# Performance work log

Measured on AMD Instinct MI355X. Metric: run time of the kernel, lower is better.

Reference implementation:

```python
import jax, jax.numpy as jnp
import numpy as np

N = 131072        # total nodes
D = 256           # d_model (params.emb_dim)
STEPS = 16        # depth steps
G = N // STEPS    # nodes per depth step (equal-sized groups)
B = 16            # batch (number of trees); all lengths equal N//B
V = 1024          # len(id2word)
# op schedule: -1 leaf embedding, -2 numeric encoder, 0/1 unary ('sin','cos'), 2/3 binary ('add','mul')
SCHEDULE = [-1, -2, 0, 2, 1, 3, 0, 2, 1, 3, 0, 2, 1, 3, 0, 2]


def setup_inputs() -> dict:
    key = jax.random.key(0)
    ks = jax.random.split(key, 8)
    tokens = jax.random.randint(ks[0], (N,), 0, V, dtype=jnp.int32)
    # children of a node at depth d must already be computed: indices < d*G
    rng = np.random.default_rng(0)
    li = np.zeros(N, np.int32)
    ri = np.zeros(N, np.int32)
    for d in range(2, STEPS):
        li[d * G:(d + 1) * G] = rng.integers(0, d * G, G)
        ri[d * G:(d + 1) * G] = rng.integers(0, d * G, G)
    depths = jnp.repeat(jnp.arange(STEPS, dtype=jnp.int32), G)
    operation_order = jnp.array(SCHEDULE, dtype=jnp.int32)
    lengths = jnp.full((B,), N // B, dtype=jnp.int32)
    s = 0.05
    leaf_table = jax.random.normal(ks[1], (V, D), jnp.float32)
    num_W1 = jax.random.normal(ks[2], (D, 1), jnp.float32) * s
    num_b1 = jnp.zeros((D,), jnp.float32)
    num_W2 = jax.random.normal(ks[3], (D, D), jnp.float32) * s
    num_b2 = jnp.zeros((D,), jnp.float32)
    una_W = jax.random.normal(ks[4], (2, 4, D, D), jnp.float32) * s
    una_b = jnp.zeros((2, 4, D), jnp.float32)
    bin_W = jax.random.normal(ks[5], (2, 10, D, D), jnp.float32) * s
    bin_b = jnp.zeros((2, 5, D), jnp.float32)
    return dict(tokens=tokens, left_idx=jnp.asarray(li), right_idx=jnp.asarray(ri),
                depths=depths, operation_order=operation_order, lengths=lengths,
                leaf_table=leaf_table, num_W1=num_W1, num_b1=num_b1,
                num_W2=num_W2, num_b2=num_b2,
                una_W=una_W, una_b=una_b, bin_W=bin_W, bin_b=bin_b)


def _unary_cell(hc, W, b):
    # hc: [G, 2, D]; W: [4, D, D] (data, forget, output, input); b: [4, D]
    h, c = hc[:, 0], hc[:, 1]
    g = jnp.einsum('nd,ked->kne', h, W) + b[:, None, :]  # y = h @ W_k.T + b_k
    i = jax.nn.sigmoid(g[0])
    f = jax.nn.sigmoid(g[1])
    o = jax.nn.sigmoid(g[2])
    u = jnp.tanh(g[3])
    c2 = i * u + f * c
    h2 = o * jnp.tanh(c2)
    h2 = h2 / jnp.linalg.norm(h2)  # global (Frobenius) norm, as in torch h.norm(p=2)
    c2 = c2 / jnp.linalg.norm(c2)
    return jnp.stack([h2, c2], axis=1)


def _binary_cell(hcl, hcr, W, b):
    # W: [10, D, D] = (data_l, data_r, f_ll, f_lr, f_rl, f_rr, out_l, out_r, in_l, in_r)
    # b: [5, D] = (data, forget_l, forget_r, output, input)
    hl, cl = hcl[:, 0], hcl[:, 1]
    hr, cr = hcr[:, 0], hcr[:, 1]
    gl = jnp.einsum('nd,ked->kne', hl, W[jnp.array([0, 2, 4, 6, 8])])
    gr = jnp.einsum('nd,ked->kne', hr, W[jnp.array([1, 3, 5, 7, 9])])
    g = gl + gr + b[:, None, :]
    i = jax.nn.sigmoid(g[0])
    f_l = jax.nn.sigmoid(g[1])
    f_r = jax.nn.sigmoid(g[2])
    o = jax.nn.sigmoid(g[3])
    u = jnp.tanh(g[4])
    c2 = i * u + f_l * cl + f_r * cr
    h2 = o * jnp.tanh(c2)
    h2 = h2 / jnp.linalg.norm(h2)
    c2 = c2 / jnp.linalg.norm(c2)
    return jnp.stack([h2, c2], axis=1)


def reference(tokens, left_idx, right_idx, depths, operation_order, lengths,
              leaf_table, num_W1, num_b1, num_W2, num_b2,
              una_W, una_b, bin_W, bin_b):
    sched = np.asarray(operation_order).tolist()  # static dispatch schedule
    n = tokens.shape[0]
    steps = len(sched)
    g = n // steps
    d_model = leaf_table.shape[1]
    acts = jnp.zeros((n, 2, d_model), leaf_table.dtype)
    for d, op in enumerate(sched):
        s = d * g
        if op == -1:  # leaf embedding with max_norm=1.0 renorm (non-differentiable scale)
            e = leaf_table[tokens[s:s + g]]
            nrm = jnp.linalg.norm(e, axis=-1, keepdims=True)
            scale = jax.lax.stop_gradient(jnp.minimum(1.0, 1.0 / (nrm + 1e-7)))
            e = e * scale
            step_act = jnp.stack([e, jnp.zeros_like(e)], axis=1)
        elif op == -2:  # numeric encoder
            x = tokens[s:s + g].astype(leaf_table.dtype)[:, None]
            h1 = jax.nn.sigmoid(x @ num_W1.T + num_b1)
            e = jax.nn.sigmoid(h1 @ num_W2.T + num_b2)
            step_act = jnp.stack([e, jnp.zeros_like(e)], axis=1)
        elif op in (0, 1):  # unary LSTM cell: gather child then cell
            child = acts[left_idx[s:s + g]]
            step_act = _unary_cell(child, una_W[op], una_b[op])
        else:  # binary LSTM cell: gather both children
            l = acts[left_idx[s:s + g]]
            r = acts[right_idx[s:s + g]]
            step_act = _binary_cell(l, r, bin_W[op - 2], bin_b[op - 2])
        acts = jax.lax.dynamic_update_slice(acts, step_act, (s, 0, 0))
    hidden = acts[:, 0, :]  # [N, D]
    batch = lengths.shape[0]
    # all lengths equal -> pad_sequence is a reshape: [B, L, D]
    return hidden.reshape(batch, n // batch, d_model)
```

## Files before the change

### kernel.cpp

```cpp
#include <hip/hip_runtime.h>
#include <hip/hip_bf16.h>
#include <cstdint>

typedef unsigned short u16;
typedef unsigned int u32;
typedef __attribute__((ext_vector_type(4))) float floatx4;
typedef __attribute__((ext_vector_type(8))) short shortx8;

#define G_STEP 8192
#define N_TOTAL 131072
#define RHALF (1280*256)

__device__ __forceinline__ float bfu2f(u16 x){ return __uint_as_float(((unsigned)x)<<16); }
__device__ __forceinline__ u16 f2bfu(float x){ __hip_bfloat16 b = __float2bfloat16(x); return *reinterpret_cast<u16*>(&b); }
__device__ __forceinline__ float sigm(float x){ return 1.0f/(1.0f+__expf(-x)); }
__device__ __forceinline__ float tanh_(float x){
  float cx = fminf(fmaxf(x,-15.f),15.f);
  float e = __expf(2.f*cx);
  return (e-1.f)/(e+1.f);
}
__device__ __forceinline__ float invs(float x){ return 1.0f/sqrtf(x); }

__device__ __forceinline__ void gl16(const void* g, void* l){
  __builtin_amdgcn_global_load_lds((const __attribute__((address_space(1))) u32*)g,
                                   (__attribute__((address_space(3))) u32*)l, 16, 0, 0);
}

template<int V> __device__ __forceinline__ void wait_vm();
template<> __device__ __forceinline__ void wait_vm<0>(){ asm volatile("s_waitcnt vmcnt(0)" ::: "memory"); }
template<> __device__ __forceinline__ void wait_vm<8>(){ asm volatile("s_waitcnt vmcnt(8)" ::: "memory"); }
template<> __device__ __forceinline__ void wait_vm<9>(){ asm volatile("s_waitcnt vmcnt(9)" ::: "memory"); }
__device__ __forceinline__ void wait_lgkm0(){ asm volatile("s_waitcnt lgkmcnt(0)" ::: "memory"); }

__device__ __forceinline__ void cvt8(const float* __restrict__ src, u16* __restrict__ dst){
  float4 a = *reinterpret_cast<const float4*>(src);
  float4 b = *reinterpret_cast<const float4*>(src+4);
  ushort4 o0; o0.x=f2bfu(a.x); o0.y=f2bfu(a.y); o0.z=f2bfu(a.z); o0.w=f2bfu(a.w);
  ushort4 o1; o1.x=f2bfu(b.x); o1.y=f2bfu(b.y); o1.z=f2bfu(b.z); o1.w=f2bfu(b.w);
  *reinterpret_cast<ushort4*>(dst)   = o0;
  *reinterpret_cast<ushort4*>(dst+4) = o1;
}

__global__ __launch_bounds__(256) void setup_kernel(
    const int* __restrict__ tokens, const float* __restrict__ leaf_table,
    const float* __restrict__ W1, const float* __restrict__ b1,
    const float* __restrict__ una_W, const float* __restrict__ bin_W,
    const float* __restrict__ num_W2,
    u16* __restrict__ wbu, u16* __restrict__ wbb, u16* __restrict__ wbn,
    u16* __restrict__ h1, u16* __restrict__ H, u16* __restrict__ C,
    float* __restrict__ sumsq)
{
  const int b = blockIdx.x, tid = threadIdx.x;
  if (b < 256){
    int row = b*8 + (tid>>5), d0 = (tid&31)*8;
    int op = row>>10, w = row&1023;
    int gate = (w>>4)&3, e = ((w>>6)<<4) | (w&15);
    cvt8(una_W + (size_t)((op*4+gate)*256 + e)*256 + d0, wbu + (size_t)row*256 + d0);
  } else if (b < 896){
    int row = (b-256)*8 + (tid>>5), d0 = (tid&31)*8;
    int ob = row / 2560, rem = row - ob*2560;
    int lr = rem / 1280, rw = rem - lr*1280;
    int eblk = rw / 80, rem2 = rw - eblk*80;
    int gate = rem2 >> 4, el = rem2 & 15;
    int e = eblk*16 + el;
    cvt8(bin_W + (size_t)((ob*10 + 2*gate + lr)*256 + e)*256 + d0, wbb + (size_t)row*256 + d0);
  } else if (b < 928){
    int row = (b-896)*8 + (tid>>5), d0 = (tid&31)*8;
    cvt8(num_W2 + (size_t)row*256 + d0, wbn + (size_t)row*256 + d0);
  } else if (b < 2976){
    int wave = tid >> 6, lane = tid & 63;
    int node = (b-928)*4 + wave;
    int t = tokens[node];
    const float4 e4 = *reinterpret_cast<const float4*>(leaf_table + (size_t)t*256 + lane*4);
    float ss = e4.x*e4.x + e4.y*e4.y + e4.z*e4.z + e4.w*e4.w;
    #pragma unroll
    for (int o = 32; o; o >>= 1) ss += __shfl_down(ss, o);
    ss = __shfl(ss, 0);
    float scale = fminf(1.0f, 1.0f/(sqrtf(ss) + 1e-7f));
    ushort4 hv;
    hv.x = f2bfu(e4.x*scale); hv.y = f2bfu(e4.y*scale);
    hv.z = f2bfu(e4.z*scale); hv.w = f2bfu(e4.w*scale);
    ushort4 zv; zv.x = zv.y = zv.z = zv.w = 0;
    *reinterpret_cast<ushort4*>(H + (size_t)node*256 + lane*4) = hv;
    *reinterpret_cast<ushort4*>(C + (size_t)node*256 + lane*4) = zv;
  } else if (b < 4000){
    int flat = (b-2976)*2048 + tid*8;
    int n = flat >> 8, d0 = flat & 255;
    float x = (float)tokens[G_STEP + n];
    float4 w0 = *reinterpret_cast<const float4*>(W1 + d0);
    float4 w1 = *reinterpret_cast<const float4*>(W1 + d0 + 4);
    float4 c0 = *reinterpret_cast<const float4*>(b1 + d0);
    float4 c1 = *reinterpret_cast<const float4*>(b1 + d0 + 4);
    ushort4 o0, o1;
    o0.x = f2bfu(sigm(x*w0.x + c0.x)); o0.y = f2bfu(sigm(x*w0.y + c0.y));
    o0.z = f2bfu(sigm(x*w0.z + c0.z)); o0.w = f2bfu(sigm(x*w0.w + c0.w));
    o1.x = f2bfu(sigm(x*w1.x + c1.x)); o1.y = f2bfu(sigm(x*w1.y + c1.y));
    o1.z = f2bfu(sigm(x*w1.z + c1.z)); o1.w = f2bfu(sigm(x*w1.w + c1.w));
    *reinterpret_cast<ushort4*>(h1 + flat)     = o0;
    *reinterpret_cast<ushort4*>(h1 + flat + 4) = o1;
  } else {
    if (tid < 32) sumsq[tid] = ((tid & 15) < 2) ? 1.0f : 0.0f;
  }
}

template<int MODE>
__global__ __launch_bounds__(256, 2) void gemm_fused(
    const u16* __restrict__ Asrc, const int* __restrict__ lidx,
    const int* __restrict__ ridx, const u16* __restrict__ Wb,
    const float* __restrict__ bias, const u16* __restrict__ Cin,
    float* __restrict__ sumsq, u16* __restrict__ H, u16* __restrict__ C,
    int sbase, int step)
{
  constexpr int NG  = (MODE==0) ? 1 : (MODE==1 ? 4 : 5);
  constexpr int NBR = (MODE==2) ? 160 : 128;
  constexpr int NT  = (MODE==2) ? 8 : 4;
  constexpr int BR  = NBR/32;
  constexpr int WN  = (MODE==2) ? 80 : 64;
  constexpr int NFR = WN/16;
  constexpr int LPS = 4 + BR;

  __shared__ u16 SA[2][128][64];
  __shared__ u16 SB[2][NBR][64];
  __shared__ float scH[16];
  __shared__ float scC[16];
  __shared__ float red[8];

  const int tid  = threadIdx.x;
  const int lane = tid & 63, wave = tid >> 6;

  const int bid = blockIdx.x;
  const int j   = bid >> 3;
  const int bx  = (bid & 7) + 8*(j & 7);
  const int by  = j >> 3;

  const int mbase = bx*128;
  const int nbase = by*NBR;
  const int l15 = lane & 15, kg = lane >> 4;
  const int rhi = lane >> 3;
  const int lc  = (lane & 7) ^ rhi;

  if (MODE != 0){
    if (tid < 16)           scH[tid]    = invs(sumsq[tid]);
    else if (tid < 32)      scC[tid-16] = invs(sumsq[tid]);
  }

  const u16* aL[4]; const u16* aR[4]; const u16* bP[BR];
  #pragma unroll
  for (int rr = 0; rr < 4; rr++){
    int r = rr*32 + wave*8 + rhi;
    int gr;
    if constexpr (MODE==0) gr = mbase + r;
    else                   gr = lidx[sbase + mbase + r];
    aL[rr] = Asrc + (size_t)gr*256 + lc*8;
    if constexpr (MODE==2)
      aR[rr] = Asrc + (size_t)ridx[sbase + mbase + r]*256 + lc*8;
  }
  #pragma unroll
  for (int rb = 0; rb < BR; rb++){
    int r = rb*32 + wave*8 + rhi;
    bP[rb] = Wb + (size_t)(nbase + r)*256 + lc*8;
  }

  floatx4 accL[4][NFR];
  #pragma unroll
  for (int i = 0; i < 4; i++)
    #pragma unroll
    for (int j2 = 0; j2 < NFR; j2++) accL[i][j2] = (floatx4)(0.0f);
  floatx4 accR[(MODE==2)?4:1][(MODE==2)?NFR:1];
  if constexpr (MODE==2){
    #pragma unroll
    for (int i = 0; i < 4; i++)
      #pragma unroll
      for (int j2 = 0; j2 < NFR; j2++) accR[i][j2] = (floatx4)(0.0f);
  }

  const int wm = (wave >> 1)*64, wn = (wave & 1)*WN;

  auto stage = [&](int t, int buf){
    const int kk = t*64;
    #pragma unroll
    for (int rr = 0; rr < 4; rr++){
      const u16* ga;
      if constexpr (MODE==2){ ga = (kk >= 256) ? aR[rr] + (kk-256) : aL[rr] + kk; }
      else                  { ga = aL[rr] + kk; }
      gl16(ga, &SA[buf][rr*32 + wave*8][0]);
    }
    #pragma unroll
    for (int rb = 0; rb < BR; rb++){
      const u16* gb;
      if constexpr (MODE==2){ gb = (kk >= 256) ? bP[rb] + RHALF + (kk-256) : bP[rb] + kk; }
      else                  { gb = bP[rb] + kk; }
      gl16(gb, &SB[buf][rb*32 + wave*8][0]);
    }
  };

  stage(0, 0);
  stage(1, 1);
  if constexpr (LPS == 8) asm volatile("s_waitcnt vmcnt(8) lgkmcnt(0)" ::: "memory");
  else                    asm volatile("s_waitcnt vmcnt(9) lgkmcnt(0)" ::: "memory");
  __builtin_amdgcn_s_barrier();

  #pragma unroll
  for (int t = 0; t < NT; t++){
    const int buf = t & 1;
    {
      shortx8 af[4], bfr[NFR];
      const int pc = (kg ^ (l15 & 7)) * 8;
      #pragma unroll
      for (int i = 0; i < 4; i++)
        af[i] = *reinterpret_cast<const shortx8*>(&SA[buf][wm + i*16 + l15][pc]);
      #pragma unroll
      for (int n = 0; n < NFR; n++)
        bfr[n] = *reinterpret_cast<const shortx8*>(&SB[buf][wn + n*16 + l15][pc]);
      if (MODE==2 && t >= 4){
        #pragma unroll
        for (int mi = 0; mi < 4; mi++)
          #pragma unroll
          for (int ni = 0; ni < NFR; ni++)
            accR[mi][ni] = __builtin_amdgcn_mfma_f32_16x16x32_bf16(af[mi], bfr[ni], accR[mi][ni], 0, 0, 0);
      } else {
        #pragma unroll
        for (int mi = 0; mi < 4; mi++)
          #pragma unroll
          for (int ni = 0; ni < NFR; ni++)
            accL[mi][ni] = __builtin_amdgcn_mfma_f32_16x16x32_bf16(af[mi], bfr[ni], accL[mi][ni], 0, 0, 0);
      }
    }
    {
      shortx8 af[4], bfr[NFR];
      const int pc = ((4 + kg) ^ (l15 & 7)) * 8;
      #pragma unroll
      for (int i = 0; i < 4; i++)
        af[i] = *reinterpret_cast<const shortx8*>(&SA[buf][wm + i*16 + l15][pc]);
      #pragma unroll
      for (int n = 0; n < NFR; n++)
        bfr[n] = *reinterpret_cast<const shortx8*>(&SB[buf][wn + n*16 + l15][pc]);
      wait_lgkm0();
      __builtin_amdgcn_s_barrier();
      if (t + 2 < NT) stage(t+2, buf);
      if (MODE==2 && t >= 4){
        #pragma unroll
        for (int mi = 0; mi < 4; mi++)
          #pragma unroll
          for (int ni = 0; ni < NFR; ni++)
            accR[mi][ni] = __builtin_amdgcn_mfma_f32_16x16x32_bf16(af[mi], bfr[ni], accR[mi][ni], 0, 0, 0);
      } else {
        #pragma unroll
        for (int mi = 0; mi < 4; mi++)
          #pragma unroll
          for (int ni = 0; ni < NFR; ni++)
            accL[mi][ni] = __builtin_amdgcn_mfma_f32_16x16x32_bf16(af[mi], bfr[ni], accL[mi][ni], 0, 0, 0);
      }
    }
    if (t + 1 < NT){
      if (t + 2 < NT) wait_vm<LPS>(); else wait_vm<0>();
      __builtin_amdgcn_s_barrier();
    }
  }

  if constexpr (MODE == 0){
    float bb[4];
    #pragma unroll
    for (int ni = 0; ni < 4; ni++) bb[ni] = bias[nbase + wn + ni*16 + l15];
    #pragma unroll
    for (int mi = 0; mi < 4; mi++){
      #pragma unroll
      for (int r = 0; r < 4; r++){
        int node = sbase + mbase + wm + mi*16 + kg*4 + r;
        u16* hp = H + (size_t)node*256 + nbase + wn + l15;
        u16* cp = C + (size_t)node*256 + nbase + wn + l15;
        #pragma unroll
        for (int ni = 0; ni < 4; ni++){
          hp[ni*16] = f2bfu(sigm(accL[mi][ni][r] + bb[ni]));
          cp[ni*16] = 0;
        }
      }
    }
  } else {
    const int eb = by*2 + (wave & 1);
    const int e  = eb*16 + l15;
    float bb[NG];
    #pragma unroll
    for (int g = 0; g < NG; g++) bb[g] = bias[g*256 + e];
    float hss = 0.f, css = 0.f;
    #pragma unroll
    for (int mi = 0; mi < 4; mi++){
      #pragma unroll
      for (int r = 0; r < 4; r++){
        int orow = mbase + wm + mi*16 + kg*4 + r;
        int node = sbase + orow;
        int chl = lidx[node];
        float sl = scH[chl >> 13];
        float cl = bfu2f(Cin[(size_t)chl*256 + e]) * scC[chl >> 13];
        float c2, h2;
        if constexpr (MODE == 1){
          float i_ = sigm(accL[mi][0][r]*sl + bb[0]);
          float f_ = sigm(accL[mi][1][r]*sl + bb[1]);
          float o_ = sigm(accL[mi][2][r]*sl + bb[2]);
          float u_ = tanh_(accL[mi][3][r]*sl + bb[3]);
          c2 = i_*u_ + f_*cl;
          h2 = o_*tanh_(c2);
        } else {
          int chr = ridx[node];
          float sr = scH[chr >> 13];
          float cr = bfu2f(Cin[(size_t)chr*256 + e]) * scC[chr >> 13];
          float g0 = accL[mi][0][r]*sl + accR[mi][0][r]*sr + bb[0];
          float g1 = accL[mi][1][r]*sl + accR[mi][1][r]*sr + bb[1];
          float g2 = accL[mi][2][r]*sl + accR[mi][2][r]*sr + bb[2];
          float g3 = accL[mi][3][r]*sl + accR[mi][3][r]*sr + bb[3];
          float g4 = accL[mi][4][r]*sl + accR[mi][4][r]*sr + bb[4];
          float i_ = sigm(g0);
          float fl = sigm(g1);
          float fr = sigm(g2);
          float o_ = sigm(g3);
          float u_ = tanh_(g4);
          c2 = i_*u_ + fl*cl + fr*cr;
          h2 = o_*tanh_(c2);
        }
        H[(size_t)node*256 + e] = f2bfu(h2);
        C[(size_t)node*256 + e] = f2bfu(c2);
        hss += h2*h2;
        css += c2*c2;
      }
    }
    #pragma unroll
    for (int o = 32; o; o >>= 1){ hss += __shfl_down(hss, o); css += __shfl_down(css, o); }
    if (lane == 0){ red[wave] = hss; red[4+wave] = css; }
    __syncthreads();
    if (tid == 0)  atomicAdd(&sumsq[step],      red[0]+red[1]+red[2]+red[3]);
    if (tid == 64) atomicAdd(&sumsq[16 + step], red[4]+red[5]+red[6]+red[7]);
  }
}

__global__ __launch_bounds__(256) void out_kernel(
    const u16* __restrict__ H, const float* __restrict__ sumsq, float* __restrict__ out)
{
  size_t base = ((size_t)blockIdx.x*256 + threadIdx.x)*8;
  int n = (int)(base >> 8);
  float s = invs(sumsq[n >> 13]);
  const uint4 v = *reinterpret_cast<const uint4*>(H + base);
  float4 o0, o1;
  o0.x = bfu2f((u16)(v.x & 0xffff))*s; o0.y = bfu2f((u16)(v.x >> 16))*s;
  o0.z = bfu2f((u16)(v.y & 0xffff))*s; o0.w = bfu2f((u16)(v.y >> 16))*s;
  o1.x = bfu2f((u16)(v.z & 0xffff))*s; o1.y = bfu2f((u16)(v.z >> 16))*s;
  o1.z = bfu2f((u16)(v.w & 0xffff))*s; o1.w = bfu2f((u16)(v.w >> 16))*s;
  *reinterpret_cast<float4*>(out + base)     = o0;
  *reinterpret_cast<float4*>(out + base + 4) = o1;
}

extern "C" void kernel_launch(void* const* d_in, const int* in_sizes, int n_in,
                              void* d_out, int out_size, void* d_ws, size_t ws_size,
                              hipStream_t stream)
{
  const int*   tokens     = (const int*)d_in[0];
  const int*   lidx       = (const int*)d_in[1];
  const int*   ridx       = (const int*)d_in[2];
  const float* leaf_table = (const float*)d_in[6];
  const float* num_W1     = (const float*)d_in[7];
  const float* num_b1     = (const float*)d_in[8];
  const float* num_W2     = (const float*)d_in[9];
  const float* num_b2     = (const float*)d_in[10];
  const float* una_W      = (const float*)d_in[11];
  const float* una_b      = (const float*)d_in[12];
  const float* bin_W      = (const float*)d_in[13];
  const float* bin_b      = (const float*)d_in[14];

  char* ws = (char*)d_ws;
  size_t off = 0;
  u16* H   = (u16*)(ws + off); off += (size_t)N_TOTAL*256*2;
  u16* wbu = (u16*)(ws + off); off += (size_t)2048*256*2;
  u16* wbb = (u16*)(ws + off); off += (size_t)5120*256*2;
  u16* wbn = (u16*)(ws + off); off += (size_t)256*256*2;
  u16* h1  = (u16*)(ws + off); off += (size_t)G_STEP*256*2;
  float* sumsq = (float*)(ws + off); off += 32*4;

  u16* C = (u16*)d_out;

  setup_kernel<<<4001, 256, 0, stream>>>(tokens, leaf_table, num_W1, num_b1,
                                         una_W, bin_W, num_W2,
                                         wbu, wbb, wbn, h1, H, C, sumsq);
  gemm_fused<0><<<128, 256, 0, stream>>>(
      h1, nullptr, nullptr, wbn, num_b2, nullptr, sumsq, H, C, G_STEP, 1);

  const int sched[16] = {-1,-2,0,2,1,3,0,2,1,3,0,2,1,3,0,2};
  for (int d = 2; d < 16; d++){
    int op = sched[d];
    int sbase = d*G_STEP;
    if (op == 0 || op == 1){
      gemm_fused<1><<<512, 256, 0, stream>>>(
          H, lidx, nullptr, wbu + (size_t)op*1024*256,
          una_b + (size_t)op*4*256, C, sumsq, H, C, sbase, d);
    } else {
      int o2 = op - 2;
      gemm_fused<2><<<512, 256, 0, stream>>>(
          H, lidx, ridx, wbb + (size_t)o2*2*1280*256,
          bin_b + (size_t)o2*5*256, C, sumsq, H, C, sbase, d);
    }
  }
  out_kernel<<<(N_TOTAL*256)/(256*8), 256, 0, stream>>>(H, sumsq, (float*)d_out);
}
```

Baseline: 369.7 us.

## Double M tile to 256 rows with 512-thread blocks sharing weight tiles

Each GEMM block now covers 256 node rows with 8 waves instead of 128 rows with 4 waves. The same B (weight) tile in LDS is reused across twice as many rows, which halves weight-tile global loads per node. Load distribution across waves, vmcnt wait counts, block swizzle, and the 8-wave reduction are reworked to match. The grid halves to 256 blocks, which may lower parallelism on a 256-CU device, and LDS per block grows.

```diff
diff --git a/kernel.cpp b/kernel.cpp
--- a/kernel.cpp
+++ b/kernel.cpp
@@ -28,8 +28,8 @@
 
 template<int V> __device__ __forceinline__ void wait_vm();
 template<> __device__ __forceinline__ void wait_vm<0>(){ asm volatile("s_waitcnt vmcnt(0)" ::: "memory"); }
-template<> __device__ __forceinline__ void wait_vm<8>(){ asm volatile("s_waitcnt vmcnt(8)" ::: "memory"); }
-template<> __device__ __forceinline__ void wait_vm<9>(){ asm volatile("s_waitcnt vmcnt(9)" ::: "memory"); }
+template<> __device__ __forceinline__ void wait_vm<6>(){ asm volatile("s_waitcnt vmcnt(6)" ::: "memory"); }
+template<> __device__ __forceinline__ void wait_vm<7>(){ asm volatile("s_waitcnt vmcnt(7)" ::: "memory"); }
 __device__ __forceinline__ void wait_lgkm0(){ asm volatile("s_waitcnt lgkmcnt(0)" ::: "memory"); }
 
 __device__ __forceinline__ void cvt8(const float* __restrict__ src, u16* __restrict__ dst){
@@ -104,7 +104,7 @@
 }
 
 template<int MODE>
-__global__ __launch_bounds__(256, 2) void gemm_fused(
+__global__ __launch_bounds__(512, 2) void gemm_fused(
     const u16* __restrict__ Asrc, const int* __restrict__ lidx,
     const int* __restrict__ ridx, const u16* __restrict__ Wb,
     const float* __restrict__ bias, const u16* __restrict__ Cin,
@@ -114,51 +114,56 @@
   constexpr int NG  = (MODE==0) ? 1 : (MODE==1 ? 4 : 5);
   constexpr int NBR = (MODE==2) ? 160 : 128;
   constexpr int NT  = (MODE==2) ? 8 : 4;
-  constexpr int BR  = NBR/32;
   constexpr int WN  = (MODE==2) ? 80 : 64;
   constexpr int NFR = WN/16;
-  constexpr int LPS = 4 + BR;
-
-  __shared__ u16 SA[2][128][64];
+  constexpr int NBG = NBR/8;
+
+  __shared__ u16 SA[2][256][64];
   __shared__ u16 SB[2][NBR][64];
   __shared__ float scH[16];
   __shared__ float scC[16];
-  __shared__ float red[8];
+  __shared__ float red[16];
 
   const int tid  = threadIdx.x;
   const int lane = tid & 63, wave = tid >> 6;
 
   const int bid = blockIdx.x;
-  const int j   = bid >> 3;
-  const int bx  = (bid & 7) + 8*(j & 7);
-  const int by  = j >> 3;
-
-  const int mbase = bx*128;
+  const int jj  = bid >> 3;
+  const int bx  = (bid & 7) + 8*(jj & 3);
+  const int by  = jj >> 2;
+  const int mbase = bx*256;
   const int nbase = by*NBR;
+
   const int l15 = lane & 15, kg = lane >> 4;
+  const int wm = (wave >> 1)*64, wn = (wave & 1)*WN;
+
+  if (MODE != 0){
+    if (tid < 16)      scH[tid]    = invs(sumsq[tid]);
+    else if (tid < 32) scC[tid-16] = invs(sumsq[tid]);
+  }
+
   const int rhi = lane >> 3;
   const int lc  = (lane & 7) ^ rhi;
 
-  if (MODE != 0){
-    if (tid < 16)           scH[tid]    = invs(sumsq[tid]);
-    else if (tid < 32)      scC[tid-16] = invs(sumsq[tid]);
-  }
-
-  const u16* aL[4]; const u16* aR[4]; const u16* bP[BR];
+  const u16* aL[4]; const u16* aR[4];
   #pragma unroll
-  for (int rr = 0; rr < 4; rr++){
-    int r = rr*32 + wave*8 + rhi;
+  for (int g = 0; g < 4; g++){
+    int r = (wave*4 + g)*8 + rhi;
     int gr;
     if constexpr (MODE==0) gr = mbase + r;
     else                   gr = lidx[sbase + mbase + r];
-    aL[rr] = Asrc + (size_t)gr*256 + lc*8;
+    aL[g] = Asrc + (size_t)gr*256 + lc*8;
     if constexpr (MODE==2)
-      aR[rr] = Asrc + (size_t)ridx[sbase + mbase + r]*256 + lc*8;
-  }
+      aR[g] = Asrc + (size_t)ridx[sbase + mbase + r]*256 + lc*8;
+  }
+  const int nbg_w = (MODE==2) ? ((wave < 4) ? 3 : 2) : 2;
+  const int bg0   = (MODE==2) ? ((wave < 4) ? wave*3 : 12 + (wave-4)*2) : wave*2;
+  const u16* bP[3];
   #pragma unroll
-  for (int rb = 0; rb < BR; rb++){
-    int r = rb*32 + wave*8 + rhi;
-    bP[rb] = Wb + (size_t)(nbase + r)*256 + lc*8;
+  for (int g = 0; g < 3; g++){
+    int gg = bg0 + g;
+    if (gg >= NBG) gg = NBG-1;
+    bP[g] = Wb + (size_t)(nbase + gg*8 + rhi)*256 + lc*8;
   }
 
   floatx4 accL[4][NFR];
@@ -174,30 +179,30 @@
       for (int j2 = 0; j2 < NFR; j2++) accR[i][j2] = (floatx4)(0.0f);
   }
 
-  const int wm = (wave >> 1)*64, wn = (wave & 1)*WN;
-
   auto stage = [&](int t, int buf){
     const int kk = t*64;
     #pragma unroll
-    for (int rr = 0; rr < 4; rr++){
+    for (int g = 0; g < 4; g++){
       const u16* ga;
-      if constexpr (MODE==2){ ga = (kk >= 256) ? aR[rr] + (kk-256) : aL[rr] + kk; }
-      else                  { ga = aL[rr] + kk; }
-      gl16(ga, &SA[buf][rr*32 + wave*8][0]);
-    }
-    #pragma unroll
-    for (int rb = 0; rb < BR; rb++){
-      const u16* gb;
-      if constexpr (MODE==2){ gb = (kk >= 256) ? bP[rb] + RHALF + (kk-256) : bP[rb] + kk; }
-      else                  { gb = bP[rb] + kk; }
-      gl16(gb, &SB[buf][rb*32 + wave*8][0]);
+      if constexpr (MODE==2){ ga = (kk >= 256) ? aR[g] + (kk-256) : aL[g] + kk; }
+      else                  { ga = aL[g] + kk; }
+      gl16(ga, &SA[buf][(wave*4 + g)*8][0]);
+    }
+    #pragma unroll
+    for (int g = 0; g < 3; g++){
+      if (g < nbg_w){
+        const u16* gb;
+        if constexpr (MODE==2){ gb = (kk >= 256) ? bP[g] + RHALF + (kk-256) : bP[g] + kk; }
+        else                  { gb = bP[g] + kk; }
+        gl16(gb, &SB[buf][(bg0 + g)*8][0]);
+      }
     }
   };
 
   stage(0, 0);
   stage(1, 1);
-  if constexpr (LPS == 8) asm volatile("s_waitcnt vmcnt(8) lgkmcnt(0)" ::: "memory");
-  else                    asm volatile("s_waitcnt vmcnt(9) lgkmcnt(0)" ::: "memory");
+  if (MODE==2 && wave < 4) asm volatile("s_waitcnt vmcnt(7) lgkmcnt(0)" ::: "memory");
+  else                     asm volatile("s_waitcnt vmcnt(6) lgkmcnt(0)" ::: "memory");
   __builtin_amdgcn_s_barrier();
 
   #pragma unroll
@@ -253,7 +258,9 @@
       }
     }
     if (t + 1 < NT){
-      if (t + 2 < NT) wait_vm<LPS>(); else wait_vm<0>();
+      if (t + 2 < NT){
+        if (MODE==2 && wave < 4) wait_vm<7>(); else wait_vm<6>();
+      } else wait_vm<0>();
       __builtin_amdgcn_s_barrier();
     }
   }
@@ -325,10 +332,20 @@
     }
     #pragma unroll
     for (int o = 32; o; o >>= 1){ hss += __shfl_down(hss, o); css += __shfl_down(css, o); }
-    if (lane == 0){ red[wave] = hss; red[4+wave] = css; }
+    if (lane == 0){ red[wave] = hss; red[8+wave] = css; }
     __syncthreads();
-    if (tid == 0)  atomicAdd(&sumsq[step],      red[0]+red[1]+red[2]+red[3]);
-    if (tid == 64) atomicAdd(&sumsq[16 + step], red[4]+red[5]+red[6]+red[7]);
+    if (tid == 0){
+      float s = 0.f;
+      #pragma unroll
+      for (int w = 0; w < 8; w++) s += red[w];
+      atomicAdd(&sumsq[step], s);
+    }
+    if (tid == 64){
+      float s = 0.f;
+      #pragma unroll
+      for (int w = 0; w < 8; w++) s += red[8+w];
+      atomicAdd(&sumsq[16 + step], s);
+    }
   }
 }
 
@@ -379,7 +396,7 @@
   setup_kernel<<<4001, 256, 0, stream>>>(tokens, leaf_table, num_W1, num_b1,
                                          una_W, bin_W, num_W2,
                                          wbu, wbb, wbn, h1, H, C, sumsq);
-  gemm_fused<0><<<128, 256, 0, stream>>>(
+  gemm_fused<0><<<64, 512, 0, stream>>>(
       h1, nullptr, nullptr, wbn, num_b2, nullptr, sumsq, H, C, G_STEP, 1);
 
   const int sched[16] = {-1,-2,0,2,1,3,0,2,1,3,0,2,1,3,0,2};
@@ -387,12 +404,12 @@
     int op = sched[d];
     int sbase = d*G_STEP;
     if (op == 0 || op == 1){
-      gemm_fused<1><<<512, 256, 0, stream>>>(
+      gemm_fused<1><<<256, 512, 0, stream>>>(
           H, lidx, nullptr, wbu + (size_t)op*1024*256,
           una_b + (size_t)op*4*256, C, sumsq, H, C, sbase, d);
     } else {
       int o2 = op - 2;
-      gemm_fused<2><<<512, 256, 0, stream>>>(
+      gemm_fused<2><<<256, 512, 0, stream>>>(
           H, lidx, ridx, wbb + (size_t)o2*2*1280*256,
           bin_b + (size_t)o2*5*256, C, sumsq, H, C, sbase, d);
     }
```

Measured after the change: 373.4 us. No clear change (+1.0%).
